# Kernel tuning notes

Measured on AMD Instinct MI355X. Metric: run time of the kernel, lower is better.

The kernel has to match this reference:

```python
import jax, jax.numpy as jnp
import numpy as np

KH = KW = 5          # deformable kernel (matches offset_channels = 2*5*5)
PAD = 2              # (5-1)//2
DG = 4               # deformable groups


def conv3d(x, w, padding, bias=None):
    # x: [N,C,D,H,W], w: [O,I,kd,kh,kw]
    out = jax.lax.conv_general_dilated(
        x, w, window_strides=(1, 1, 1), padding=padding,
        dimension_numbers=('NCDHW', 'OIDHW', 'NCDHW'))
    if bias is not None:
        out = out + bias[None, :, None, None, None]
    return out


def deform_conv2d(x, offset, weight, pad=PAD, dg=DG):
    """torchvision/mmcv-style deformable conv, stride 1, groups=1, no bias.
    x: [N,C,H,W]; offset: [N, dg*2*K, H, W] ordered (group, k, (dy,dx));
    weight: [Cout, C, KH, KW]."""
    N, C, H, W = x.shape
    K = KH * KW
    off = offset.reshape(N, dg, K, 2, H, W)
    ky, kx = jnp.meshgrid(jnp.arange(KH), jnp.arange(KW), indexing='ij')
    ky = ky.reshape(K).astype(x.dtype)
    kx = kx.reshape(K).astype(x.dtype)
    # absolute sampling positions: [N,dg,K,H,W]
    base_y = ky[:, None, None] - pad + jnp.arange(H, dtype=x.dtype)[None, :, None]
    base_x = kx[:, None, None] - pad + jnp.arange(W, dtype=x.dtype)[None, None, :]
    sy = base_y[None, None] + off[:, :, :, 0]
    sx = base_x[None, None] + off[:, :, :, 1]
    y0 = jnp.floor(sy)
    x0 = jnp.floor(sx)
    wy = sy - y0
    wx = sx - x0
    y0i = y0.astype(jnp.int32)
    x0i = x0.astype(jnp.int32)
    Cg = C // dg
    xg = x.reshape(N, dg, Cg, H * W)

    def gather(yi, xi):
        valid = (yi >= 0) & (yi < H) & (xi >= 0) & (xi < W)
        yc = jnp.clip(yi, 0, H - 1)
        xc = jnp.clip(xi, 0, W - 1)
        idx = (yc * W + xc).reshape(N, dg, 1, K * H * W)
        v = jnp.take_along_axis(xg, idx, axis=3).reshape(N, dg, Cg, K, H, W)
        return v * valid[:, :, None].astype(x.dtype)

    v00 = gather(y0i, x0i)
    v01 = gather(y0i, x0i + 1)
    v10 = gather(y0i + 1, x0i)
    v11 = gather(y0i + 1, x0i + 1)
    wy_ = wy[:, :, None]
    wx_ = wx[:, :, None]
    samp = (v00 * (1 - wy_) * (1 - wx_) + v01 * (1 - wy_) * wx_
            + v10 * wy_ * (1 - wx_) + v11 * wy_ * wx_)
    samp = samp.reshape(N, C, K, H, W)             # deform groups only affect offsets
    wmat = weight.reshape(weight.shape[0], C, K)
    return jnp.einsum('nckhw,ock->nohw', samp, wmat)


def setup_inputs() -> dict:
    key = jax.random.key(0)
    k0, k1, k2, k3, k4 = jax.random.split(key, 5)
    bs, C, T, H, W = 1, 256, 4, 48, 48
    x = jax.random.normal(k0, (bs, C, T, H, W), dtype=jnp.float32)
    # spatio_offset: Conv3d(C -> dg*2*K, kernel (1,5,5), pad (0,2,2), no bias)
    w_off = jax.random.normal(k1, (DG * 2 * KH * KW, C, 1, KH, KW), dtype=jnp.float32) * 0.01
    # spatio_adaption: DeformConv2d weight, init std=0.01 (per init_weights)
    w_def = jax.random.normal(k2, (C, C, KH, KW), dtype=jnp.float32) * 0.01
    # temporal: Conv3d(C -> C, kernel (3,3,3), pad (1,1,1), with bias)
    fan_in = C * 27
    w_temp = jax.random.normal(k3, (C, C, 3, 3, 3), dtype=jnp.float32) * (1.0 / np.sqrt(fan_in))
    b_temp = jax.random.normal(k4, (C,), dtype=jnp.float32) * 0.01
    return {'x': x, 'w_off': w_off, 'w_def': w_def, 'w_temp': w_temp, 'b_temp': b_temp}


def reference(x, w_off, w_def, w_temp, b_temp):
    bs, C, T, H, W = x.shape
    # offset branch uses detached input (torch: x.detach())
    offset = conv3d(jax.lax.stop_gradient(x), w_off, [(0, 0), (PAD, PAD), (PAD, PAD)])
    off_fold = offset.transpose(0, 2, 1, 3, 4).reshape(bs * T, -1, H, W)
    x_fold = x.transpose(0, 2, 1, 3, 4).reshape(bs * T, C, H, W)
    x_spatio_fold = deform_conv2d(x_fold, off_fold, w_def)
    x_spatio = x_spatio_fold.reshape(bs, T, C, H, W).transpose(0, 2, 1, 3, 4)
    # cascaded=False branch: temporal conv on original x, then residual sum
    x_temporal = conv3d(x, w_temp, [(1, 1), (1, 1), (1, 1)], b_temp)
    return x_spatio + x_temporal
```

## Files before the change

kernel.cpp:

```cpp
#include <hip/hip_runtime.h>
#include <hip/hip_bf16.h>

#define T    4
#define C    256
#define H    48
#define W    48
#define HW   2304
#define OFFC 200
#define CK5  6400
#define CK9  2304
#define NFULL 9216
#define BPAD 72

typedef __attribute__((ext_vector_type(8))) short bf16x8;
typedef __attribute__((ext_vector_type(4))) float f32x4;

__device__ __forceinline__ unsigned short f2bf(float f) {
    unsigned int u = __float_as_uint(f);
    return (unsigned short)((u + 0x7FFFu + ((u >> 16) & 1u)) >> 16);
}
__device__ __forceinline__ float bflo(unsigned int v) { return __uint_as_float(v << 16); }
__device__ __forceinline__ float bfhi(unsigned int v) { return __uint_as_float(v & 0xFFFF0000u); }
__device__ __forceinline__ unsigned int pack2(float lo, float hi) {
    __hip_bfloat162 h = __float22bfloat162_rn(make_float2(lo, hi));
    return *reinterpret_cast<unsigned int*>(&h);
}
__device__ __forceinline__ void gload16(const void* g, void* l) {
    __builtin_amdgcn_global_load_lds(
        (const __attribute__((address_space(1))) unsigned int*)g,
        (__attribute__((address_space(3))) unsigned int*)l, 16, 0, 0);
}

__global__ __launch_bounds__(256) void prep_k(const float* __restrict__ w_off,
                                              const float* __restrict__ w_def,
                                              const float* __restrict__ w_temp,
                                              const float* __restrict__ bias,
                                              unsigned short* __restrict__ wbo,
                                              unsigned short* __restrict__ wbd,
                                              unsigned short* __restrict__ wbT,
                                              float* __restrict__ offb,
                                              float* __restrict__ out) {
    long i = (long)blockIdx.x * 256 + threadIdx.x;
    if (i < 1638400) {
        const int c = (int)(i & 255); const int rest = (int)(i >> 8);
        const int q = rest % 25, o = rest / 25;
        wbo[(long)o * CK5 + q * 256 + c] =
            (o < OFFC) ? f2bf(w_off[((long)o * 256 + c) * 25 + q]) : (unsigned short)0;
    } else if (i < 3276800) {
        i -= 1638400;
        const int c = (int)(i & 255); const int rest = (int)(i >> 8);
        const int q = rest % 25, o = rest / 25;
        wbd[(long)o * CK5 + q * 256 + c] = f2bf(w_def[((long)o * 256 + c) * 25 + q]);
    } else if (i < 5046272) {
        i -= 3276800;
        const int c = (int)(i & 255); const int rest = (int)(i >> 8);
        const int j = rest % 9, oo = rest / 9;
        const int o = oo & 255, kt = oo >> 8;
        wbT[(long)kt * (256 * CK9) + (long)o * CK9 + j * 256 + c] =
            f2bf(w_temp[((long)o * 256 + c) * 27 + kt * 9 + j]);
    } else if (i < 5636096) {
        i -= 5046272;
        ((float4*)offb)[i] = make_float4(0.f, 0.f, 0.f, 0.f);
    } else {
        i -= 5636096;
        const float b = bias[(int)(i / 2304)];
        ((float4*)out)[i] = make_float4(b, b, b, b);
    }
}

__global__ __launch_bounds__(256) void xt_k(const float* __restrict__ x,
                                            unsigned short* __restrict__ xt) {
    __shared__ float tile[64][65];
    const int p0 = blockIdx.x * 64, c0 = blockIdx.y * 64, t = blockIdx.z;
    const int px = threadIdx.x & 63, sub = threadIdx.x >> 6;
    for (int cl = sub; cl < 64; cl += 4)
        tile[px][cl] = x[((long)(c0 + cl) * T + t) * HW + p0 + px];
    __syncthreads();
    const int seg = sub * 16;
    unsigned int pk[8];
    #pragma unroll
    for (int d = 0; d < 8; ++d)
        pk[d] = pack2(tile[px][seg + d * 2], tile[px][seg + d * 2 + 1]);
    unsigned short* orow = xt + ((long)t * HW + p0 + px) * 256 + c0 + seg;
    *(uint4*)(orow + 0) = make_uint4(pk[0], pk[1], pk[2], pk[3]);
    *(uint4*)(orow + 8) = make_uint4(pk[4], pk[5], pk[6], pk[7]);
}

__device__ __forceinline__ void mfma_iter(const unsigned short* __restrict__ Asl,
                                          const unsigned short* __restrict__ Bsl,
                                          int wave, int quad, int l16, f32x4 acc[4][2]) {
    const int wm = (wave & 1) * 64, wn = (wave >> 1) * 32;
    #pragma unroll
    for (int kh = 0; kh < 2; ++kh) {
        bf16x8 af[4], bfr[2];
        #pragma unroll
        for (int i = 0; i < 4; ++i) {
            const int row = wm + i * 16 + l16;
            const int slot = (kh * 4 + quad + (l16 & 7)) & 7;
            af[i] = *(const bf16x8*)(Asl + row * 64 + slot * 8);
        }
        #pragma unroll
        for (int j = 0; j < 2; ++j)
            bfr[j] = *(const bf16x8*)(Bsl + (wn + j * 16 + l16) * BPAD + kh * 32 + quad * 8);
        #pragma unroll
        for (int i = 0; i < 4; ++i)
            #pragma unroll
            for (int j = 0; j < 2; ++j)
                acc[i][j] = __builtin_amdgcn_mfma_f32_16x16x32_bf16(af[i], bfr[j], acc[i][j], 0, 0, 0);
    }
}
__device__ __forceinline__ void epilogue_atomic(float* __restrict__ Cf, int m0, int n0,
                                                int wave, int quad, int l16,
                                                int Mvalid, f32x4 acc[4][2]) {
    const int wm = (wave & 1) * 64, wn = (wave >> 1) * 32;
    #pragma unroll
    for (int i = 0; i < 4; ++i)
        #pragma unroll
        for (int rr = 0; rr < 4; ++rr) {
            const int o = m0 + wm + i * 16 + quad * 4 + rr;
            if (o >= Mvalid) continue;
            #pragma unroll
            for (int j = 0; j < 2; ++j)
                unsafeAtomicAdd(Cf + (long)o * NFULL + n0 + wn + j * 16 + l16, acc[i][j][rr]);
        }
}

__device__ __forceinline__ void gemm_shift_body(unsigned short* __restrict__ Asl,
                                                unsigned short* __restrict__ Bsl,
                                                const unsigned short* __restrict__ A, long ldA,
                                                const unsigned short* __restrict__ xt, int tsrc,
                                                float* __restrict__ Cf, int Mvalid,
                                                int m0, int n0, int k0, int iters, int mode) {
    const int tid = threadIdx.x;
    const int wave = tid >> 6, lane = tid & 63;
    const int quad = lane >> 4, l16 = lane & 15;
    const int t = n0 / HW, p0 = n0 - t * HW;
    const int px = tid >> 2, seg = tid & 3;
    const int p = p0 + px, h = p / 48, w = p - h * 48;
    const unsigned short* xts = xt + (long)tsrc * HW * 256 + seg * 8;

    const int r8 = lane >> 3, s8 = lane & 7;
    const int qg = (s8 - r8) & 7;
    const long ldAb = ldA * 2;
    const char* Ap = (const char*)A + (long)(m0 + wave * 32 + r8) * ldAb
                     + (long)k0 * 2 + qg * 16;
    const long rstep8 = 8 * ldAb;
    unsigned short* la = Asl + wave * 2048;

    auto produce = [&](int kk, uint4& v0, uint4& v1) {
        const int q = kk >> 8, cb = kk & 255;
        int qy, qx;
        if (mode == 0) { const int d = q / 5; qy = d - 2; qx = q - d * 5 - 2; }
        else           { const int d = q / 3; qy = d - 1; qx = q - d * 3 - 1; }
        const int y = h + qy, xx = w + qx;
        v0 = make_uint4(0u, 0u, 0u, 0u); v1 = v0;
        if ((y >= 0) & (y < 48) & (xx >= 0) & (xx < 48)) {
            const unsigned short* bp = xts + (y * 48 + xx) * 256 + cb;
            v0 = *(const uint4*)bp; v1 = *(const uint4*)(bp + 32);
        }
    };

    uint4 cv0, cv1;
    produce(k0, cv0, cv1);

    f32x4 acc[4][2] = {};
    for (int i = 0; i < iters; ++i) {
        __syncthreads();
        #pragma unroll
        for (int c2 = 0; c2 < 4; ++c2) gload16(Ap + c2 * rstep8, la + c2 * 512);
        Ap += 128;
        *(uint4*)(Bsl + px * BPAD + seg * 8)      = cv0;
        *(uint4*)(Bsl + px * BPAD + 32 + seg * 8) = cv1;
        __syncthreads();
        if (i + 1 < iters) produce(k0 + (i + 1) * 64, cv0, cv1);
        mfma_iter(Asl, Bsl, wave, quad, l16, acc);
    }
    epilogue_atomic(Cf, m0, n0, wave, quad, l16, Mvalid, acc);
}

__global__ __launch_bounds__(256, 4) void gemm_ot_k(const unsigned short* __restrict__ wbo,
                                                    const unsigned short* __restrict__ wbT,
                                                    const unsigned short* __restrict__ xt,
                                                    float* __restrict__ offb,
                                                    float* __restrict__ out) {
    __shared__ unsigned short Asl[128 * 64];
    __shared__ unsigned short Bsl[64 * BPAD];
    const int z = blockIdx.z, n0 = blockIdx.x * 64, m0 = blockIdx.y * 128;
    const int t = n0 / HW;
    if (z < 4) {
        gemm_shift_body(Asl, Bsl, wbo, CK5, xt, t, offb, OFFC, m0, n0, z * 1600, 25, 0);
    } else {
        const int zz = z - 4, kt = zz >> 1, half = zz & 1;
        const int tsrc = t + kt - 1;
        if (tsrc < 0 || tsrc >= T) return;
        gemm_shift_body(Asl, Bsl, wbT + (long)kt * 256 * CK9, CK9, xt, tsrc, out, C,
                        m0, n0, half * 1152, 18, 1);
    }
}

__device__ __forceinline__ void pos_calc(int h, int w, int q, float dy, float dx,
                                         float wgt[4], int idx[4]) {
    const int d = q / 5;
    const int qy = d - 2, qx = q - d * 5 - 2;
    const float sy = (float)(h + qy) + dy;
    const float sx = (float)(w + qx) + dx;
    const float y0f = floorf(sy), x0f = floorf(sx);
    const float wy = sy - y0f, wx = sx - x0f;
    const int y0 = (int)y0f, x0 = (int)x0f;
    const int y1 = y0 + 1, x1 = x0 + 1;
    float w00 = (1.f - wy) * (1.f - wx);
    float w01 = (1.f - wy) * wx;
    float w10 = wy * (1.f - wx);
    float w11 = wy * wx;
    const bool vy0 = (y0 >= 0) & (y0 < 48), vy1 = (y1 >= 0) & (y1 < 48);
    const bool vx0 = (x0 >= 0) & (x0 < 48), vx1 = (x1 >= 0) & (x1 < 48);
    if (!(vy0 & vx0)) w00 = 0.f;
    if (!(vy0 & vx1)) w01 = 0.f;
    if (!(vy1 & vx0)) w10 = 0.f;
    if (!(vy1 & vx1)) w11 = 0.f;
    const int yc0 = min(max(y0, 0), 47), yc1 = min(max(y1, 0), 47);
    const int xc0 = min(max(x0, 0), 47), xc1 = min(max(x1, 0), 47);
    wgt[0] = w00; wgt[1] = w01; wgt[2] = w10; wgt[3] = w11;
    idx[0] = yc0 * 48 + xc0; idx[1] = yc0 * 48 + xc1;
    idx[2] = yc1 * 48 + xc0; idx[3] = yc1 * 48 + xc1;
}
__device__ __forceinline__ uint4 blend4(const uint4 u[4], const float wgt[4]) {
    unsigned int pk[4];
    #pragma unroll
    for (int qi = 0; qi < 4; ++qi) {
        const unsigned int a = ((const unsigned int*)&u[0])[qi];
        const unsigned int b = ((const unsigned int*)&u[1])[qi];
        const unsigned int c = ((const unsigned int*)&u[2])[qi];
        const unsigned int d = ((const unsigned int*)&u[3])[qi];
        const float rl = wgt[0] * bflo(a) + wgt[1] * bflo(b) + wgt[2] * bflo(c) + wgt[3] * bflo(d);
        const float rh = wgt[0] * bfhi(a) + wgt[1] * bfhi(b) + wgt[2] * bfhi(c) + wgt[3] * bfhi(d);
        pk[qi] = pack2(rl, rh);
    }
    return make_uint4(pk[0], pk[1], pk[2], pk[3]);
}

__global__ __launch_bounds__(256, 4) void gemm_def_k(const unsigned short* __restrict__ A,
                                                     const unsigned short* __restrict__ xt,
                                                     const float* __restrict__ offb,
                                                     float* __restrict__ Cf) {
    __shared__ unsigned short Asl[128 * 64];
    __shared__ unsigned short Bsl[64 * BPAD];
    const int tid = threadIdx.x;
    const int wave = tid >> 6, lane = tid & 63;
    const int quad = lane >> 4, l16 = lane & 15;
    const int n0 = blockIdx.x * 64, m0 = blockIdx.y * 128, k0 = blockIdx.z * 1600;
    const int t = n0 / HW, p0 = n0 - t * HW;
    const int px = tid >> 2, seg = tid & 3;
    const int p = p0 + px, h = p / 48, w = p - h * 48;
    const int nabs = n0 + px;
    const unsigned short* xts = xt + (long)t * HW * 256 + seg * 8;

    const int r8 = lane >> 3, s8 = lane & 7;
    const int qg = (s8 - r8) & 7;
    const long ldAb = (long)CK5 * 2;
    const char* Ap = (const char*)A + (long)(m0 + wave * 32 + r8) * ldAb
                     + (long)k0 * 2 + qg * 16;
    const long rstep8 = 8 * ldAb;
    unsigned short* la = Asl + wave * 2048;

    auto off_load = [&](int kk, float& dy, float& dx) {
        const int q = kk >> 8, g = (kk & 255) >> 6;
        dy = offb[(long)(g * 50 + 2 * q) * NFULL + nabs];
        dx = offb[(long)(g * 50 + 2 * q + 1) * NFULL + nabs];
    };
    auto corners = [&](int kk, float dy, float dx, uint4 u[8], float wgt[4]) {
        const int cb = kk & 255;
        int idx[4];
        pos_calc(h, w, kk >> 8, dy, dx, wgt, idx);
        #pragma unroll
        for (int cn = 0; cn < 4; ++cn) {
            const unsigned short* bp = xts + idx[cn] * 256 + cb;
            u[cn]     = *(const uint4*)bp;
            u[cn + 4] = *(const uint4*)(bp + 32);
        }
    };

    uint4 pkv0, pkv1;
    float dyN, dxN;
    {
        float dy0, dx0;
        off_load(k0, dy0, dx0);
        uint4 u[8]; float wg[4];
        corners(k0, dy0, dx0, u, wg);
        pkv0 = blend4(u, wg);
        pkv1 = blend4(u + 4, wg);
        off_load(k0 + 64, dyN, dxN);
    }

    f32x4 acc[4][2] = {};
    for (int i = 0; i < 25; ++i) {
        const int kk = k0 + i * 64;
        __syncthreads();
        #pragma unroll
        for (int c2 = 0; c2 < 4; ++c2) gload16(Ap + c2 * rstep8, la + c2 * 512);
        Ap += 128;
        *(uint4*)(Bsl + px * BPAD + seg * 8)      = pkv0;
        *(uint4*)(Bsl + px * BPAD + 32 + seg * 8) = pkv1;
        __syncthreads();
        const bool more = (i + 1 < 25);
        uint4 u[8]; float wg[4];
        if (more) {
            corners(kk + 64, dyN, dxN, u, wg);
            if (i + 2 < 25) off_load(kk + 128, dyN, dxN);
        }
        mfma_iter(Asl, Bsl, wave, quad, l16, acc);
        if (more) {
            pkv0 = blend4(u, wg);
            pkv1 = blend4(u + 4, wg);
        }
    }
    epilogue_atomic(Cf, m0, n0, wave, quad, l16, C, acc);
}

extern "C" void kernel_launch(void* const* d_in, const int* in_sizes, int n_in,
                              void* d_out, int out_size, void* d_ws, size_t ws_size,
                              hipStream_t stream) {
    const float* x      = (const float*)d_in[0];
    const float* w_off  = (const float*)d_in[1];
    const float* w_def  = (const float*)d_in[2];
    const float* w_temp = (const float*)d_in[3];
    const float* b_temp = (const float*)d_in[4];
    float* out = (float*)d_out;

    unsigned short* xt   = (unsigned short*)d_ws;
    float*          offb = (float*)((char*)d_ws + 4718592ul);
    unsigned short* wbo  = (unsigned short*)((char*)d_ws + 14155776ul);
    unsigned short* wbd  = (unsigned short*)((char*)d_ws + 17432576ul);
    unsigned short* wbT  = (unsigned short*)((char*)d_ws + 20709376ul);

    prep_k<<<24320, 256, 0, stream>>>(w_off, w_def, w_temp, b_temp, wbo, wbd, wbT, offb, out);
    xt_k<<<dim3(36, 4, T), 256, 0, stream>>>(x, xt);
    gemm_ot_k<<<dim3(144, 2, 10), 256, 0, stream>>>(wbo, wbT, xt, offb, out);
    gemm_def_k<<<dim3(144, 2, 4), 256, 0, stream>>>(wbd, xt, offb, out);
}
```

Before: 303.6 us.

## Move temporal conv into deform kernel, widen offset GEMM tile, fuse prep launches

Folds the x transpose kernel into the weight-prep launch, which removes one kernel launch. The offset conv becomes its own kernel with a 128x128 tile and a 5-way K split, giving more reuse per block. The temporal conv now runs inside the same launch as the deformable GEMM, so that launch has work that does not depend on the offsets. This reduces the serial dependency and improves occupancy balance, but the offset GEMM now runs alone with fewer blocks and more accumulator registers.

Result: faster. 289.3 us (-4.7%).

```diff
diff --git a/kernel.cpp b/kernel.cpp
--- a/kernel.cpp
+++ b/kernel.cpp
@@ -31,15 +31,35 @@
         (__attribute__((address_space(3))) unsigned int*)l, 16, 0, 0);
 }
 
-__global__ __launch_bounds__(256) void prep_k(const float* __restrict__ w_off,
-                                              const float* __restrict__ w_def,
-                                              const float* __restrict__ w_temp,
-                                              const float* __restrict__ bias,
-                                              unsigned short* __restrict__ wbo,
-                                              unsigned short* __restrict__ wbd,
-                                              unsigned short* __restrict__ wbT,
-                                              float* __restrict__ offb,
-                                              float* __restrict__ out) {
+__global__ __launch_bounds__(256) void prep_xt_k(const float* __restrict__ x,
+                                                 const float* __restrict__ w_off,
+                                                 const float* __restrict__ w_def,
+                                                 const float* __restrict__ w_temp,
+                                                 const float* __restrict__ bias,
+                                                 unsigned short* __restrict__ wbo,
+                                                 unsigned short* __restrict__ wbd,
+                                                 unsigned short* __restrict__ wbT,
+                                                 float* __restrict__ offb,
+                                                 float* __restrict__ out,
+                                                 unsigned short* __restrict__ xt) {
+    __shared__ float tile[64][65];
+    if (blockIdx.x >= 24320) {
+        const int zb = blockIdx.x - 24320;
+        const int p0 = (zb % 36) * 64, c0 = ((zb / 36) & 3) * 64, t = zb / 144;
+        const int px = threadIdx.x & 63, sub = threadIdx.x >> 6;
+        for (int cl = sub; cl < 64; cl += 4)
+            tile[px][cl] = x[((long)(c0 + cl) * T + t) * HW + p0 + px];
+        __syncthreads();
+        const int seg = sub * 16;
+        unsigned int pk[8];
+        #pragma unroll
+        for (int d = 0; d < 8; ++d)
+            pk[d] = pack2(tile[px][seg + d * 2], tile[px][seg + d * 2 + 1]);
+        unsigned short* orow = xt + ((long)t * HW + p0 + px) * 256 + c0 + seg;
+        *(uint4*)(orow + 0) = make_uint4(pk[0], pk[1], pk[2], pk[3]);
+        *(uint4*)(orow + 8) = make_uint4(pk[4], pk[5], pk[6], pk[7]);
+        return;
+    }
     long i = (long)blockIdx.x * 256 + threadIdx.x;
     if (i < 1638400) {
         const int c = (int)(i & 255); const int rest = (int)(i >> 8);
@@ -68,24 +88,6 @@
     }
 }
 
-__global__ __launch_bounds__(256) void xt_k(const float* __restrict__ x,
-                                            unsigned short* __restrict__ xt) {
-    __shared__ float tile[64][65];
-    const int p0 = blockIdx.x * 64, c0 = blockIdx.y * 64, t = blockIdx.z;
-    const int px = threadIdx.x & 63, sub = threadIdx.x >> 6;
-    for (int cl = sub; cl < 64; cl += 4)
-        tile[px][cl] = x[((long)(c0 + cl) * T + t) * HW + p0 + px];
-    __syncthreads();
-    const int seg = sub * 16;
-    unsigned int pk[8];
-    #pragma unroll
-    for (int d = 0; d < 8; ++d)
-        pk[d] = pack2(tile[px][seg + d * 2], tile[px][seg + d * 2 + 1]);
-    unsigned short* orow = xt + ((long)t * HW + p0 + px) * 256 + c0 + seg;
-    *(uint4*)(orow + 0) = make_uint4(pk[0], pk[1], pk[2], pk[3]);
-    *(uint4*)(orow + 8) = make_uint4(pk[4], pk[5], pk[6], pk[7]);
-}
-
 __device__ __forceinline__ void mfma_iter(const unsigned short* __restrict__ Asl,
                                           const unsigned short* __restrict__ Bsl,
                                           int wave, int quad, int l16, f32x4 acc[4][2]) {
@@ -125,77 +127,85 @@
         }
 }
 
-__device__ __forceinline__ void gemm_shift_body(unsigned short* __restrict__ Asl,
-                                                unsigned short* __restrict__ Bsl,
-                                                const unsigned short* __restrict__ A, long ldA,
-                                                const unsigned short* __restrict__ xt, int tsrc,
-                                                float* __restrict__ Cf, int Mvalid,
-                                                int m0, int n0, int k0, int iters, int mode) {
+__global__ __launch_bounds__(256, 4) void gemm_off_k(const unsigned short* __restrict__ A,
+                                                     const unsigned short* __restrict__ xt,
+                                                     float* __restrict__ Cf) {
+    __shared__ unsigned short Asl[128 * 64];
+    __shared__ unsigned short Bsl[128 * BPAD];
     const int tid = threadIdx.x;
     const int wave = tid >> 6, lane = tid & 63;
     const int quad = lane >> 4, l16 = lane & 15;
+    const int n0 = blockIdx.x * 128, m0 = blockIdx.y * 128, k0 = blockIdx.z * 1280;
     const int t = n0 / HW, p0 = n0 - t * HW;
-    const int px = tid >> 2, seg = tid & 3;
-    const int p = p0 + px, h = p / 48, w = p - h * 48;
-    const unsigned short* xts = xt + (long)tsrc * HW * 256 + seg * 8;
+    const int wm = (wave & 1) * 64, wn = (wave >> 1) * 64;
 
     const int r8 = lane >> 3, s8 = lane & 7;
     const int qg = (s8 - r8) & 7;
-    const long ldAb = ldA * 2;
+    const long ldAb = (long)CK5 * 2;
     const char* Ap = (const char*)A + (long)(m0 + wave * 32 + r8) * ldAb
                      + (long)k0 * 2 + qg * 16;
     const long rstep8 = 8 * ldAb;
     unsigned short* la = Asl + wave * 2048;
 
-    auto produce = [&](int kk, uint4& v0, uint4& v1) {
+    const int px = tid >> 1, half = tid & 1;
+    const int p = p0 + px, h = p / 48, w = p - h * 48;
+    const unsigned short* xts = xt + (long)t * HW * 256 + half * 32;
+
+    auto produce = [&](int kk, uint4 v[4]) {
         const int q = kk >> 8, cb = kk & 255;
-        int qy, qx;
-        if (mode == 0) { const int d = q / 5; qy = d - 2; qx = q - d * 5 - 2; }
-        else           { const int d = q / 3; qy = d - 1; qx = q - d * 3 - 1; }
-        const int y = h + qy, xx = w + qx;
-        v0 = make_uint4(0u, 0u, 0u, 0u); v1 = v0;
+        const int d = q / 5;
+        const int y = h + d - 2, xx = w + (q - d * 5) - 2;
+        v[0] = make_uint4(0u, 0u, 0u, 0u); v[1] = v[0]; v[2] = v[0]; v[3] = v[0];
         if ((y >= 0) & (y < 48) & (xx >= 0) & (xx < 48)) {
             const unsigned short* bp = xts + (y * 48 + xx) * 256 + cb;
-            v0 = *(const uint4*)bp; v1 = *(const uint4*)(bp + 32);
+            #pragma unroll
+            for (int d4 = 0; d4 < 4; ++d4) v[d4] = *(const uint4*)(bp + d4 * 8);
         }
     };
 
-    uint4 cv0, cv1;
-    produce(k0, cv0, cv1);
-
-    f32x4 acc[4][2] = {};
-    for (int i = 0; i < iters; ++i) {
+    uint4 cv[4];
+    produce(k0, cv);
+
+    f32x4 acc[4][4] = {};
+    for (int i = 0; i < 20; ++i) {
         __syncthreads();
         #pragma unroll
         for (int c2 = 0; c2 < 4; ++c2) gload16(Ap + c2 * rstep8, la + c2 * 512);
         Ap += 128;
-        *(uint4*)(Bsl + px * BPAD + seg * 8)      = cv0;
-        *(uint4*)(Bsl + px * BPAD + 32 + seg * 8) = cv1;
-        __syncthreads();
-        if (i + 1 < iters) produce(k0 + (i + 1) * 64, cv0, cv1);
-        mfma_iter(Asl, Bsl, wave, quad, l16, acc);
-    }
-    epilogue_atomic(Cf, m0, n0, wave, quad, l16, Mvalid, acc);
-}
-
-__global__ __launch_bounds__(256, 4) void gemm_ot_k(const unsigned short* __restrict__ wbo,
-                                                    const unsigned short* __restrict__ wbT,
-                                                    const unsigned short* __restrict__ xt,
-                                                    float* __restrict__ offb,
-                                                    float* __restrict__ out) {
-    __shared__ unsigned short Asl[128 * 64];
-    __shared__ unsigned short Bsl[64 * BPAD];
-    const int z = blockIdx.z, n0 = blockIdx.x * 64, m0 = blockIdx.y * 128;
-    const int t = n0 / HW;
-    if (z < 4) {
-        gemm_shift_body(Asl, Bsl, wbo, CK5, xt, t, offb, OFFC, m0, n0, z * 1600, 25, 0);
-    } else {
-        const int zz = z - 4, kt = zz >> 1, half = zz & 1;
-        const int tsrc = t + kt - 1;
-        if (tsrc < 0 || tsrc >= T) return;
-        gemm_shift_body(Asl, Bsl, wbT + (long)kt * 256 * CK9, CK9, xt, tsrc, out, C,
-                        m0, n0, half * 1152, 18, 1);
-    }
+        #pragma unroll
+        for (int d4 = 0; d4 < 4; ++d4)
+            *(uint4*)(Bsl + px * BPAD + half * 32 + d4 * 8) = cv[d4];
+        __syncthreads();
+        if (i + 1 < 20) produce(k0 + (i + 1) * 64, cv);
+        #pragma unroll
+        for (int kh = 0; kh < 2; ++kh) {
+            bf16x8 af[4], bfr[4];
+            #pragma unroll
+            for (int ii = 0; ii < 4; ++ii) {
+                const int row = wm + ii * 16 + l16;
+                const int slot = (kh * 4 + quad + (l16 & 7)) & 7;
+                af[ii] = *(const bf16x8*)(Asl + row * 64 + slot * 8);
+            }
+            #pragma unroll
+            for (int j = 0; j < 4; ++j)
+                bfr[j] = *(const bf16x8*)(Bsl + (wn + j * 16 + l16) * BPAD + kh * 32 + quad * 8);
+            #pragma unroll
+            for (int ii = 0; ii < 4; ++ii)
+                #pragma unroll
+                for (int j = 0; j < 4; ++j)
+                    acc[ii][j] = __builtin_amdgcn_mfma_f32_16x16x32_bf16(af[ii], bfr[j], acc[ii][j], 0, 0, 0);
+        }
+    }
+    #pragma unroll
+    for (int i = 0; i < 4; ++i)
+        #pragma unroll
+        for (int rr = 0; rr < 4; ++rr) {
+            const int o = m0 + wm + i * 16 + quad * 4 + rr;
+            if (o >= OFFC) continue;
+            #pragma unroll
+            for (int j = 0; j < 4; ++j)
+                unsafeAtomicAdd(Cf + (long)o * NFULL + n0 + wn + j * 16 + l16, acc[i][j][rr]);
+        }
 }
 
 __device__ __forceinline__ void pos_calc(int h, int w, int q, float dy, float dx,
@@ -239,16 +249,16 @@
     return make_uint4(pk[0], pk[1], pk[2], pk[3]);
 }
 
-__global__ __launch_bounds__(256, 4) void gemm_def_k(const unsigned short* __restrict__ A,
-                                                     const unsigned short* __restrict__ xt,
-                                                     const float* __restrict__ offb,
-                                                     float* __restrict__ Cf) {
-    __shared__ unsigned short Asl[128 * 64];
-    __shared__ unsigned short Bsl[64 * BPAD];
+__device__ __forceinline__ void gemm_def_body(unsigned short* __restrict__ Asl,
+                                              unsigned short* __restrict__ Bsl,
+                                              const unsigned short* __restrict__ A,
+                                              const unsigned short* __restrict__ xt,
+                                              const float* __restrict__ offb,
+                                              float* __restrict__ Cf,
+                                              int m0, int n0, int k0) {
     const int tid = threadIdx.x;
     const int wave = tid >> 6, lane = tid & 63;
     const int quad = lane >> 4, l16 = lane & 15;
-    const int n0 = blockIdx.x * 64, m0 = blockIdx.y * 128, k0 = blockIdx.z * 1600;
     const int t = n0 / HW, p0 = n0 - t * HW;
     const int px = tid >> 2, seg = tid & 3;
     const int p = p0 + px, h = p / 48, w = p - h * 48;
@@ -317,6 +327,76 @@
     epilogue_atomic(Cf, m0, n0, wave, quad, l16, C, acc);
 }
 
+__device__ __forceinline__ void gemm_temp_body(unsigned short* __restrict__ Asl,
+                                               unsigned short* __restrict__ Bsl,
+                                               const unsigned short* __restrict__ A,
+                                               const unsigned short* __restrict__ xt, int tsrc,
+                                               float* __restrict__ Cf,
+                                               int m0, int n0, int k0) {
+    const int tid = threadIdx.x;
+    const int wave = tid >> 6, lane = tid & 63;
+    const int quad = lane >> 4, l16 = lane & 15;
+    const int t = n0 / HW, p0 = n0 - t * HW;
+    const int px = tid >> 2, seg = tid & 3;
+    const int p = p0 + px, h = p / 48, w = p - h * 48;
+    const unsigned short* xts = xt + (long)tsrc * HW * 256 + seg * 8;
+
+    const int r8 = lane >> 3, s8 = lane & 7;
+    const int qg = (s8 - r8) & 7;
+    const long ldAb = (long)CK9 * 2;
+    const char* Ap = (const char*)A + (long)(m0 + wave * 32 + r8) * ldAb
+                     + (long)k0 * 2 + qg * 16;
+    const long rstep8 = 8 * ldAb;
+    unsigned short* la = Asl + wave * 2048;
+
+    auto produce = [&](int kk, uint4& v0, uint4& v1) {
+        const int q = kk >> 8, cb = kk & 255;
+        const int d = q / 3;
+        const int y = h + d - 1, xx = w + (q - d * 3) - 1;
+        v0 = make_uint4(0u, 0u, 0u, 0u); v1 = v0;
+        if ((y >= 0) & (y < 48) & (xx >= 0) & (xx < 48)) {
+            const unsigned short* bp = xts + (y * 48 + xx) * 256 + cb;
+            v0 = *(const uint4*)bp; v1 = *(const uint4*)(bp + 32);
+        }
+    };
+
+    uint4 cv0, cv1;
+    produce(k0, cv0, cv1);
+
+    f32x4 acc[4][2] = {};
+    for (int i = 0; i < 18; ++i) {
+        __syncthreads();
+        #pragma unroll
+        for (int c2 = 0; c2 < 4; ++c2) gload16(Ap + c2 * rstep8, la + c2 * 512);
+        Ap += 128;
+        *(uint4*)(Bsl + px * BPAD + seg * 8)      = cv0;
+        *(uint4*)(Bsl + px * BPAD + 32 + seg * 8) = cv1;
+        __syncthreads();
+        if (i + 1 < 18) produce(k0 + (i + 1) * 64, cv0, cv1);
+        mfma_iter(Asl, Bsl, wave, quad, l16, acc);
+    }
+    epilogue_atomic(Cf, m0, n0, wave, quad, l16, C, acc);
+}
+
+__global__ __launch_bounds__(256, 4) void gemm_dt_k(const unsigned short* __restrict__ wbd,
+                                                    const unsigned short* __restrict__ wbT,
+                                                    const unsigned short* __restrict__ xt,
+                                                    const float* __restrict__ offb,
+                                                    float* __restrict__ out) {
+    __shared__ unsigned short Asl[128 * 64];
+    __shared__ unsigned short Bsl[64 * BPAD];
+    const int z = blockIdx.z, n0 = blockIdx.x * 64, m0 = blockIdx.y * 128;
+    if (z < 4) {
+        gemm_def_body(Asl, Bsl, wbd, xt, offb, out, m0, n0, z * 1600);
+    } else {
+        const int zz = z - 4, kt = zz >> 1, half = zz & 1;
+        const int t = n0 / HW, tsrc = t + kt - 1;
+        if (tsrc < 0 || tsrc >= T) return;
+        gemm_temp_body(Asl, Bsl, wbT + (long)kt * 256 * CK9, xt, tsrc, out,
+                       m0, n0, half * 1152);
+    }
+}
+
 extern "C" void kernel_launch(void* const* d_in, const int* in_sizes, int n_in,
                               void* d_out, int out_size, void* d_ws, size_t ws_size,
                               hipStream_t stream) {
@@ -333,8 +413,8 @@
     unsigned short* wbd  = (unsigned short*)((char*)d_ws + 17432576ul);
     unsigned short* wbT  = (unsigned short*)((char*)d_ws + 20709376ul);
 
-    prep_k<<<24320, 256, 0, stream>>>(w_off, w_def, w_temp, b_temp, wbo, wbd, wbT, offb, out);
-    xt_k<<<dim3(36, 4, T), 256, 0, stream>>>(x, xt);
-    gemm_ot_k<<<dim3(144, 2, 10), 256, 0, stream>>>(wbo, wbT, xt, offb, out);
-    gemm_def_k<<<dim3(144, 2, 4), 256, 0, stream>>>(wbd, xt, offb, out);
-}
+    prep_xt_k<<<24896, 256, 0, stream>>>(x, w_off, w_def, w_temp, b_temp,
+                                         wbo, wbd, wbT, offb, out, xt);
+    gemm_off_k<<<dim3(72, 2, 5), 256, 0, stream>>>(wbo, xt, offb);
+    gemm_dt_k<<<dim3(144, 2, 10), 256, 0, stream>>>(wbd, wbT, xt, offb, out);
+}
```
